# Optimization experiments

Measured on AMD Instinct MI355X. Metric: run time of the kernel, lower is better.

Reference implementation:

```python
import jax, jax.numpy as jnp
import numpy as np

N_R, N_S, D, L = 20000, 5000, 512, 3

def setup_inputs() -> dict:
    key = jax.random.key(0)
    ks = jax.random.split(key, 7)
    s = 1.0 / np.sqrt(D)  # xavier-ish scale to keep activations bounded
    return {
        "h_s": jax.random.normal(ks[0], (N_S, D), jnp.float32),
        "A_rs": jax.random.uniform(ks[1], (N_R, N_S), jnp.float32),
        "r_embed": jax.random.normal(ks[2], (N_R, D), jnp.float32) * s,
        "Wr": jax.random.normal(ks[3], (L, D, D), jnp.float32) * s,  # reading self-transform per layer
        "Ws": jax.random.normal(ks[4], (L, D, D), jnp.float32) * s,  # skill->reading cross-transform
        "Vr": jax.random.normal(ks[5], (L, D, D), jnp.float32) * s,  # reading->skill cross-transform
        "Vs": jax.random.normal(ks[6], (L, D, D), jnp.float32) * s,  # skill self-transform
    }

def reference(h_s, A_rs, r_embed, Wr, Ws, Vr, Vs):
    # ReadingGCNStage.forward: h = dropout(r_embed.weight) (eval-mode no-op),
    # then BipartiteGCNStack(h_s, h, A_rs): per-layer degree-normalized bipartite
    # message passing with dense per-side transforms and ReLU.
    eps = 1e-6
    deg_r = A_rs.sum(axis=1, keepdims=True) + eps   # [N_R, 1] reading degrees
    deg_s = A_rs.sum(axis=0)[:, None] + eps          # [N_S, 1] skill degrees
    h_r = r_embed
    for l in range(Wr.shape[0]):  # fixed small n_layers
        m_r = (A_rs @ h_s) / deg_r        # [N_R, D] mean-aggregated skill msgs
        m_s = (A_rs.T @ h_r) / deg_s      # [N_S, D] mean-aggregated reading msgs
        h_r_new = jax.nn.relu(m_r @ Ws[l] + h_r @ Wr[l])
        h_s = jax.nn.relu(m_s @ Vr[l] + h_s @ Vs[l])
        h_r = h_r_new
    return h_r  # updated reading embeddings [N_R, D]
```

## Files before the change

### kernel.cpp

```cpp
#include <hip/hip_runtime.h>


typedef __bf16 bf16_t;
typedef __attribute__((ext_vector_type(8))) __bf16 bf16x8;
typedef __attribute__((ext_vector_type(4))) __bf16 bf16x4;
typedef __attribute__((ext_vector_type(4))) float f32x4;

#define N_R 20000
#define N_S 5000
#define DD  512
#define MR_PAD 20224
#define MS_PAD 5120
#define KS_PAD 5056
#define KR_PAD 20224

__device__ __forceinline__ void gll16(const bf16_t* g, bf16_t* l) {
  __builtin_amdgcn_global_load_lds(
      (const __attribute__((address_space(1))) void*)g,
      (__attribute__((address_space(3))) void*)l, 16, 0, 0);
}


__global__ __launch_bounds__(256) void conv_rowsum_A(
    const float* __restrict__ A, bf16_t* __restrict__ Ab, float* __restrict__ deg_r) {
  int r = blockIdx.x;
  int t = threadIdx.x;
  __shared__ float wsum[4];
  if (r < N_R) {
    const float4* Arow = (const float4*)(A + (size_t)r * N_S);
    float s = 0.f;
    for (int c4 = t; c4 < N_S / 4; c4 += 256) {
      float4 v = Arow[c4];
      s += v.x + v.y + v.z + v.w;
      bf16x4 pv;
      pv[0] = (bf16_t)v.x; pv[1] = (bf16_t)v.y; pv[2] = (bf16_t)v.z; pv[3] = (bf16_t)v.w;
      *(bf16x4*)(Ab + (size_t)r * KS_PAD + 4 * c4) = pv;
    }
    if (t < KS_PAD - N_S) Ab[(size_t)r * KS_PAD + N_S + t] = (bf16_t)0.f;
    for (int off = 32; off > 0; off >>= 1) s += __shfl_down(s, off, 64);
    if ((t & 63) == 0) wsum[t >> 6] = s;
    __syncthreads();
    if (t == 0) deg_r[r] = wsum[0] + wsum[1] + wsum[2] + wsum[3] + 1e-6f;
  } else {
    for (int c = t; c < KS_PAD; c += 256) Ab[(size_t)r * KS_PAD + c] = (bf16_t)0.f;
  }
}

__global__ void init_deg_s(float* __restrict__ deg_s) {
  int i = blockIdx.x * 256 + threadIdx.x;
  if (i < N_S) deg_s[i] = 1e-6f;
}

__global__ __launch_bounds__(256) void transpose_A_deg(
    const bf16_t* __restrict__ Ab, bf16_t* __restrict__ At, float* __restrict__ deg_s) {
  __shared__ float tile[64][65];
  __shared__ float csum[4][64];
  int rt = blockIdx.x * 64;
  int st = blockIdx.y * 64;
  int tx = threadIdx.x & 63;
  int ty = threadIdx.x >> 6;
  int s = st + tx;
  float part = 0.f;
  for (int i = 0; i < 16; ++i) {
    int rr = ty * 16 + i;
    int r = rt + rr;
    float v = 0.f;
    if (r < N_R && s < KS_PAD) v = (float)Ab[(size_t)r * KS_PAD + s];
    tile[rr][tx] = v;
    part += v;
  }
  csum[ty][tx] = part;
  __syncthreads();
  if (ty == 0 && s < N_S)
    atomicAdd(&deg_s[s], csum[0][tx] + csum[1][tx] + csum[2][tx] + csum[3][tx]);
  for (int i = 0; i < 16; ++i) {
    int rr = ty * 16 + i;
    int r = rt + tx;
    if (r < KR_PAD) At[(size_t)(st + rr) * KR_PAD + r] = (bf16_t)tile[tx][rr];
  }
}

template <typename SrcT>
__global__ __launch_bounds__(256) void transpose_to_bf16(
    const SrcT* __restrict__ src, int R, int C, bf16_t* __restrict__ dst, int ldd) {
  __shared__ float tile[64][65];
  int rt = blockIdx.x * 64;
  int ct = blockIdx.y * 64;
  int tx = threadIdx.x & 63;
  int ty = threadIdx.x >> 6;
  for (int i = 0; i < 16; ++i) {
    int rr = ty * 16 + i;
    int r = rt + rr;
    float v = 0.f;
    if (r < R) v = (float)src[(size_t)r * C + ct + tx];
    tile[rr][tx] = v;
  }
  __syncthreads();
  for (int i = 0; i < 16; ++i) {
    int rr = ty * 16 + i;
    int r = rt + tx;
    if (r < ldd) dst[(size_t)(ct + rr) * ldd + r] = (bf16_t)tile[tx][rr];
  }
}

__global__ __launch_bounds__(256) void transpose_weights(
    const float* __restrict__ Wr, const float* __restrict__ Ws,
    const float* __restrict__ Vr, const float* __restrict__ Vs,
    bf16_t* __restrict__ WT) {
  int z = blockIdx.z;
  int t4 = z & 3, l = z >> 2;
  const float* srcs[4] = {Wr, Ws, Vr, Vs};
  const float* src = srcs[t4] + (size_t)l * DD * DD;
  bf16_t* dst = WT + (size_t)z * DD * DD;
  __shared__ float tile[64][65];
  int rt = blockIdx.x * 64, ct = blockIdx.y * 64;
  int tx = threadIdx.x & 63, ty = threadIdx.x >> 6;
  for (int i = 0; i < 16; ++i) {
    int rr = ty * 16 + i;
    tile[rr][tx] = src[(size_t)(rt + rr) * DD + ct + tx];
  }
  __syncthreads();
  for (int i = 0; i < 16; ++i) {
    int rr = ty * 16 + i;
    dst[(size_t)(ct + rr) * DD + rt + tx] = (bf16_t)tile[tx][rr];
  }
}

__global__ __launch_bounds__(256) void conv_pad(
    const float* __restrict__ src, bf16_t* __restrict__ dst, int R, int Rp) {
  size_t i = (size_t)blockIdx.x * 256 + threadIdx.x;
  size_t tot = (size_t)Rp * DD;
  if (i < tot) {
    int r = (int)(i / DD);
    dst[i] = (r < R) ? (bf16_t)src[i] : (bf16_t)0.f;
  }
}

__global__ __launch_bounds__(256) void combine_div(
    const float* __restrict__ part, int S, size_t stride,
    const float* __restrict__ deg, int Mreal, int Mpad, bf16_t* __restrict__ out) {
  size_t base = ((size_t)blockIdx.x * 256 + threadIdx.x) * 4;
  if (base >= (size_t)Mpad * DD) return;
  f32x4 s = *(const f32x4*)(part + base);
  for (int k = 1; k < S; ++k) s += *(const f32x4*)(part + (size_t)k * stride + base);
  int r = (int)(base >> 9);
  float inv = (r < Mreal) ? 1.0f / deg[r] : 0.f;
  bf16x4 o;
  o[0] = (bf16_t)(s[0] * inv); o[1] = (bf16_t)(s[1] * inv);
  o[2] = (bf16_t)(s[2] * inv); o[3] = (bf16_t)(s[3] * inv);
  *(bf16x4*)(out + base) = o;
}

__global__ __launch_bounds__(512, 2) void gemm256(
    const bf16_t* __restrict__ A, const bf16_t* __restrict__ B, int ld,
    int kt_total, int kt_chunk, float* __restrict__ Cpart, size_t part_stride) {
  __shared__ bf16_t As[2][256 * 64];
  __shared__ bf16_t Bs[2][256 * 64];
  const int tid = threadIdx.x;
  const int lane = tid & 63;
  const int wave = tid >> 6;
  const int bid = blockIdx.x;
  const int m0 = (bid >> 1) * 256;
  const int n0 = (bid & 1) * 256;
  const int z = blockIdx.y;
  const int ktb = z * kt_chunk;
  int kte = ktb + kt_chunk;
  if (kte > kt_total) kte = kt_total;
  if (ktb >= kte) return;
  const int wm = (wave >> 2) * 128;
  const int wn = (wave & 3) * 64;
  const int lr = lane & 15;
  const int quad = lane >> 4;
  const int rloc = lane >> 3;
  const int cel = ((lane & 7) ^ rloc) * 8;

  auto SA = [&](int b, int q, int t) {
    int k0 = (t < kte ? t : kte - 1) * 64;
    gll16(A + (size_t)(m0 + q * 64 + wave * 8 + rloc) * ld + k0 + cel,
          &As[b][(q * 64 + wave * 8) * 64]);
  };
  auto SB = [&](int b, int q, int t) {
    int k0 = (t < kte ? t : kte - 1) * 64;
    gll16(B + (size_t)(n0 + q * 64 + wave * 8 + rloc) * ld + k0 + cel,
          &Bs[b][(q * 64 + wave * 8) * 64]);
  };

  f32x4 acc[8][4] = {};
  bf16x8 af[4], bf[4];

#define PHASE(BUF, MH, KS, READB, ...)                                           \
  {                                                                              \
    _Pragma("unroll")                                                            \
    for (int i = 0; i < 4; ++i) {                                                \
      int r = wm + (MH) * 64 + i * 16 + lr;                                      \
      af[i] = *(const bf16x8*)&As[BUF][r * 64 +                                  \
                                       (((KS) * 32 + quad * 8) ^ ((r & 7) * 8))];\
    }                                                                            \
    if (READB) {                                                                 \
      _Pragma("unroll")                                                          \
      for (int j = 0; j < 4; ++j) {                                              \
        int r = wn + j * 16 + lr;                                                \
        bf[j] = *(const bf16x8*)&Bs[BUF][r * 64 +                                \
                                       (((KS) * 32 + quad * 8) ^ ((r & 7) * 8))];\
      }                                                                          \
    }                                                                            \
    __VA_ARGS__;                                                                 \
    __builtin_amdgcn_s_barrier();                                                \
    asm volatile("s_waitcnt lgkmcnt(0)" ::: "memory");                           \
    __builtin_amdgcn_s_setprio(1);                                               \
    _Pragma("unroll")                                                            \
    for (int i = 0; i < 4; ++i)                                                  \
      _Pragma("unroll")                                                          \
      for (int j = 0; j < 4; ++j)                                                \
        acc[(MH) * 4 + i][j] = __builtin_amdgcn_mfma_f32_16x16x32_bf16(          \
            af[i], bf[j], acc[(MH) * 4 + i][j], 0, 0, 0);                        \
    __builtin_amdgcn_s_setprio(0);                                               \
  }

  SB(0, 0, ktb); SB(0, 1, ktb); SB(0, 2, ktb); SB(0, 3, ktb);
  SA(0, 0, ktb); SA(0, 2, ktb);
  SA(0, 1, ktb); SA(0, 3, ktb);
  SB(1, 0, ktb + 1); SB(1, 1, ktb + 1);
  asm volatile("s_waitcnt vmcnt(4)" ::: "memory");
  __builtin_amdgcn_s_barrier();

  const int nt = kte - ktb;
  for (int ti = 0; ti < nt; ++ti) {
    const int t = ktb + ti;
    const int buf = ti & 1;
    const int nb = buf ^ 1;
    PHASE(buf, 0, 0, 1, SB(nb, 2, t + 1); SB(nb, 3, t + 1));
    asm volatile("s_waitcnt vmcnt(4)" ::: "memory");
    __builtin_amdgcn_s_barrier();
    PHASE(buf, 1, 0, 0, SA(nb, 0, t + 1); SA(nb, 2, t + 1));
    __builtin_amdgcn_s_barrier();
    PHASE(buf, 0, 1, 1, SA(nb, 1, t + 1); SA(nb, 3, t + 1));
    __builtin_amdgcn_s_barrier();
    PHASE(buf, 1, 1, 0, SB(buf, 0, t + 2); SB(buf, 1, t + 2));
    asm volatile("s_waitcnt vmcnt(4)" ::: "memory");
    __builtin_amdgcn_s_barrier();
  }
  asm volatile("s_waitcnt vmcnt(0)" ::: "memory");
#undef PHASE

  float* P = Cpart + (size_t)z * part_stride;
#pragma unroll
  for (int ii = 0; ii < 8; ++ii)
#pragma unroll
    for (int j = 0; j < 4; ++j) {
      int c = n0 + wn + j * 16 + lr;
#pragma unroll
      for (int g = 0; g < 4; ++g) {
        int r = m0 + wm + ii * 16 + quad * 4 + g;
        P[(size_t)r * DD + c] = acc[ii][j][g];
      }
    }
}

template <bool HAS2, int EPI>
__global__ __launch_bounds__(256) void gemm64(
    const bf16_t* __restrict__ A1, const bf16_t* __restrict__ B1, int kt1, int lda1, int ldb1,
    const bf16_t* __restrict__ A2, const bf16_t* __restrict__ B2, int kt2, int lda2, int ldb2,
    int kt_chunk,
    bf16_t* __restrict__ Cb, int Mreal, const float* __restrict__ deg,
    float* __restrict__ Cf, float* __restrict__ Cpart, size_t part_stride) {
  __shared__ bf16_t As[2 * 128 * 32];
  __shared__ bf16_t Bs[2 * 128 * 32];
  const int tid = threadIdx.x;
  const int lane = tid & 63;
  const int wave = tid >> 6;
  const int m0 = blockIdx.x * 128;
  const int n0 = blockIdx.y * 128;
  const int lrow = lane >> 2;
  const int lcol = (lane & 3) * 8;
  const int wm = (wave >> 1) * 64;
  const int wn = (wave & 1) * 64;
  const int lr = lane & 15;
  const int quad = lane >> 4;

  f32x4 acc[4][4] = {};

  const int ktot = kt1 + (HAS2 ? kt2 : 0);
  const int ktb = blockIdx.z * kt_chunk;
  const int kte = (ktb + kt_chunk < ktot) ? ktb + kt_chunk : ktot;

  for (int kt = ktb; kt < kte; ++kt) {
    const bf16_t* Ap; const bf16_t* Bp; int lda, ldb, k0;
    if (!HAS2 || kt < kt1) { Ap = A1; Bp = B1; lda = lda1; ldb = ldb1; k0 = kt * 64; }
    else                   { Ap = A2; Bp = B2; lda = lda2; ldb = ldb2; k0 = (kt - kt1) * 64; }
#pragma unroll
    for (int g = 0; g < 4; ++g) {
      const int h = g >> 1;
      const int rb = (g & 1) * 64 + wave * 16;
      gll16(Ap + (size_t)(m0 + rb + lrow) * lda + k0 + h * 32 + lcol,
            &As[h * 4096 + rb * 32]);
      gll16(Bp + (size_t)(n0 + rb + lrow) * ldb + k0 + h * 32 + lcol,
            &Bs[h * 4096 + rb * 32]);
    }
    __syncthreads();
    bf16x8 af[2][4], bq[2][4];
#pragma unroll
    for (int h = 0; h < 2; ++h)
#pragma unroll
      for (int i = 0; i < 4; ++i) {
        af[h][i] = *(const bf16x8*)&As[h * 4096 + (wm + i * 16 + lr) * 32 + quad * 8];
        bq[h][i] = *(const bf16x8*)&Bs[h * 4096 + (wn + i * 16 + lr) * 32 + quad * 8];
      }
#pragma unroll
    for (int h = 0; h < 2; ++h)
#pragma unroll
      for (int i = 0; i < 4; ++i)
#pragma unroll
        for (int j = 0; j < 4; ++j)
          acc[i][j] = __builtin_amdgcn_mfma_f32_16x16x32_bf16(af[h][i], bq[h][j], acc[i][j], 0, 0, 0);
    __syncthreads();
  }

  if (EPI == 2) {
    float* P = Cpart + blockIdx.z * part_stride;
#pragma unroll
    for (int i = 0; i < 4; ++i)
#pragma unroll
      for (int j = 0; j < 4; ++j) {
        int c = n0 + wn + j * 16 + lr;
#pragma unroll
        for (int g = 0; g < 4; ++g) {
          int r = m0 + wm + i * 16 + quad * 4 + g;
          P[(size_t)r * DD + c] = acc[i][j][g];
        }
      }
  } else {
#pragma unroll
    for (int i = 0; i < 4; ++i)
#pragma unroll
      for (int j = 0; j < 4; ++j) {
        int c = n0 + wn + j * 16 + lr;
#pragma unroll
        for (int g = 0; g < 4; ++g) {
          int r = m0 + wm + i * 16 + quad * 4 + g;
          if (r < Mreal) {
            float v = acc[i][j][g];
            if (EPI == 0) v /= deg[r];
            else v = fmaxf(v, 0.f);
            Cb[(size_t)r * DD + c] = (bf16_t)v;
            if (EPI == 1 && Cf != nullptr) Cf[(size_t)r * DD + c] = v;
          }
        }
      }
  }
}

extern "C" void kernel_launch(void* const* d_in, const int* in_sizes, int n_in,
                              void* d_out, int out_size, void* d_ws, size_t ws_size,
                              hipStream_t stream) {
  const float* h_s0 = (const float*)d_in[0];
  const float* A    = (const float*)d_in[1];
  const float* r_em = (const float*)d_in[2];
  const float* Wr   = (const float*)d_in[3];
  const float* Ws   = (const float*)d_in[4];
  const float* Vr   = (const float*)d_in[5];
  const float* Vs   = (const float*)d_in[6];
  float* out = (float*)d_out;

  char* p = (char*)d_ws;
  auto alloc = [&](size_t bytes) {
    char* q = p;
    p += (bytes + 255) & ~(size_t)255;
    return q;
  };
  bf16_t* Ab  = (bf16_t*)alloc((size_t)MR_PAD * KS_PAD * 2);
  bf16_t* At  = (bf16_t*)alloc((size_t)MS_PAD * KR_PAD * 2);
  bf16_t* hsT = (bf16_t*)alloc((size_t)DD * KS_PAD * 2);
  bf16_t* hrT = (bf16_t*)alloc((size_t)DD * KR_PAD * 2);
  bf16_t* WT  = (bf16_t*)alloc((size_t)12 * DD * DD * 2);
  bf16_t* hs_b[2] = {(bf16_t*)alloc((size_t)MS_PAD * DD * 2), (bf16_t*)alloc((size_t)MS_PAD * DD * 2)};
  bf16_t* hr_b[2] = {(bf16_t*)alloc((size_t)MR_PAD * DD * 2), (bf16_t*)alloc((size_t)MR_PAD * DD * 2)};
  bf16_t* mr_b = (bf16_t*)alloc((size_t)MR_PAD * DD * 2);
  bf16_t* ms_b = (bf16_t*)alloc((size_t)MS_PAD * DD * 2);
  float* deg_r = (float*)alloc((size_t)N_R * 4);
  float* deg_s = (float*)alloc((size_t)N_S * 4);
  size_t core_bytes = (size_t)(p - (char*)d_ws);
  size_t part_stride_r = (size_t)MR_PAD * DD;
  size_t part_stride_s = (size_t)MS_PAD * DD;
  size_t part_bytes = (part_stride_r * 3 > part_stride_s * 6 ? part_stride_r * 3 : part_stride_s * 6) * 4;
  bool split_ok = (core_bytes + part_bytes + 256 <= ws_size);
  float* part = split_ok ? (float*)alloc(part_bytes) : nullptr;
  if (core_bytes > ws_size) return;

  conv_rowsum_A<<<MR_PAD, 256, 0, stream>>>(A, Ab, deg_r);
  init_deg_s<<<(N_S + 255) / 256, 256, 0, stream>>>(deg_s);
  transpose_A_deg<<<dim3(316, 80), 256, 0, stream>>>(Ab, At, deg_s);
  transpose_to_bf16<float><<<dim3(79, 8), 256, 0, stream>>>(h_s0, N_S, DD, hsT, KS_PAD);
  transpose_to_bf16<float><<<dim3(316, 8), 256, 0, stream>>>(r_em, N_R, DD, hrT, KR_PAD);
  transpose_weights<<<dim3(8, 8, 12), 256, 0, stream>>>(Wr, Ws, Vr, Vs, WT);
  conv_pad<<<(MS_PAD * DD) / 256, 256, 0, stream>>>(h_s0, hs_b[0], N_S, MS_PAD);
  conv_pad<<<(MR_PAD * DD) / 256, 256, 0, stream>>>(r_em, hr_b[0], N_R, MR_PAD);

  const int ktA = KS_PAD / 64;
  const int ktT = KR_PAD / 64;

  int cur = 0;
  for (int l = 0; l < 3; ++l) {
    bf16_t* WrT = WT + ((size_t)l * 4 + 0) * DD * DD;
    bf16_t* WsT = WT + ((size_t)l * 4 + 1) * DD * DD;
    bf16_t* VrT = WT + ((size_t)l * 4 + 2) * DD * DD;
    bf16_t* VsT = WT + ((size_t)l * 4 + 3) * DD * DD;

    if (split_ok) {
      gemm256<<<dim3(79 * 2, 3), 512, 0, stream>>>(
          Ab, hsT, KS_PAD, ktA, 27, part, part_stride_r);
      combine_div<<<MR_PAD * DD / 1024, 256, 0, stream>>>(
          part, 3, part_stride_r, deg_r, N_R, MR_PAD, mr_b);
    } else {
      gemm64<false, 0><<<dim3(158, 4, 1), 256, 0, stream>>>(
          Ab, hsT, ktA, KS_PAD, KS_PAD, nullptr, nullptr, 0, 0, 0,
          ktA, mr_b, N_R, deg_r, nullptr, nullptr, 0);
    }
    if (l < 2) {
      if (split_ok) {
        gemm256<<<dim3(20 * 2, 6), 512, 0, stream>>>(
            At, hrT, KR_PAD, ktT, 53, part, part_stride_s);
        combine_div<<<MS_PAD * DD / 1024, 256, 0, stream>>>(
            part, 6, part_stride_s, deg_s, N_S, MS_PAD, ms_b);
      } else {
        gemm64<false, 0><<<dim3(40, 4, 1), 256, 0, stream>>>(
            At, hrT, ktT, KR_PAD, KR_PAD, nullptr, nullptr, 0, 0, 0,
            ktT, ms_b, N_S, deg_s, nullptr, nullptr, 0);
      }
    }
    gemm64<true, 1><<<dim3(158, 4, 1), 256, 0, stream>>>(
        mr_b, WsT, 8, DD, DD, hr_b[cur], WrT, 8, DD, DD,
        16, hr_b[1 - cur], N_R, nullptr, (l == 2) ? out : nullptr, nullptr, 0);
    if (l < 2) {
      gemm64<true, 1><<<dim3(40, 4, 1), 256, 0, stream>>>(
          ms_b, VrT, 8, DD, DD, hs_b[cur], VsT, 8, DD, DD,
          16, hs_b[1 - cur], N_S, nullptr, nullptr, nullptr, 0);
      transpose_to_bf16<bf16_t><<<dim3(316, 8), 256, 0, stream>>>(hr_b[1 - cur], N_R, DD, hrT, KR_PAD);
      transpose_to_bf16<bf16_t><<<dim3(79, 8), 256, 0, stream>>>(hs_b[1 - cur], N_S, DD, hsT, KS_PAD);
    }
    cur = 1 - cur;
  }
}
```

Baseline: 1.868 ms.

## Merge paired GEMM/transposes into combined launches and store split-K partials in bf16

Pairs the reading-side and skill-side work of each layer into single launches: one grouped split-K GEMM kernel, one combine kernel, one dual dense-transform GEMM, and one transpose kernel. This cuts launch count and lets the small skill-side work fill the GPU alongside the reading side. Split-K partials are now written as bf16 instead of fp32, halving partial traffic at some accuracy cost. The transposes are vectorised to 16-byte loads and stores, and the init and pad kernels are merged. The fallback path for small workspaces is removed.

```diff
diff --git a/kernel.cpp b/kernel.cpp
--- a/kernel.cpp
+++ b/kernel.cpp
@@ -46,61 +46,114 @@
   }
 }
 
-__global__ void init_deg_s(float* __restrict__ deg_s) {
-  int i = blockIdx.x * 256 + threadIdx.x;
-  if (i < N_S) deg_s[i] = 1e-6f;
+__global__ __launch_bounds__(256) void conv_pad2(
+    const float* __restrict__ r_em, bf16_t* __restrict__ hr0,
+    const float* __restrict__ h_s0, bf16_t* __restrict__ hs0,
+    float* __restrict__ deg_s) {
+  size_t i = (size_t)blockIdx.x * 256 + threadIdx.x;
+  const size_t totR = (size_t)MR_PAD * DD;
+  const size_t totS = (size_t)MS_PAD * DD;
+  if (i < totR) {
+    int r = (int)(i >> 9);
+    hr0[i] = (r < N_R) ? (bf16_t)r_em[i] : (bf16_t)0.f;
+  } else if (i < totR + totS) {
+    size_t j = i - totR;
+    int r = (int)(j >> 9);
+    hs0[j] = (r < N_S) ? (bf16_t)h_s0[j] : (bf16_t)0.f;
+  } else {
+    size_t j = i - totR - totS;
+    if (j < N_S) deg_s[j] = 1e-6f;
+  }
 }
 
 __global__ __launch_bounds__(256) void transpose_A_deg(
     const bf16_t* __restrict__ Ab, bf16_t* __restrict__ At, float* __restrict__ deg_s) {
   __shared__ float tile[64][65];
-  __shared__ float csum[4][64];
   int rt = blockIdx.x * 64;
   int st = blockIdx.y * 64;
-  int tx = threadIdx.x & 63;
-  int ty = threadIdx.x >> 6;
-  int s = st + tx;
-  float part = 0.f;
-  for (int i = 0; i < 16; ++i) {
-    int rr = ty * 16 + i;
+  int t = threadIdx.x;
+  const bool inA = (st < KS_PAD);
+  int row = t >> 3;
+  int c = (t & 7) * 8;
+#pragma unroll
+  for (int k = 0; k < 2; ++k) {
+    int rr = row + k * 32;
+    if (inA) {
+      bf16x8 v = *(const bf16x8*)(Ab + (size_t)(rt + rr) * KS_PAD + st + c);
+#pragma unroll
+      for (int j = 0; j < 8; ++j) tile[rr][c + j] = (float)v[j];
+    } else {
+#pragma unroll
+      for (int j = 0; j < 8; ++j) tile[rr][c + j] = 0.f;
+    }
+  }
+  __syncthreads();
+  if (t < 64 && inA && st + t < N_S) {
+    float s = 0.f;
+#pragma unroll 8
+    for (int r = 0; r < 64; ++r) s += tile[r][t];
+    atomicAdd(&deg_s[st + t], s);
+  }
+  int sl = t >> 2;
+  int r0 = (t & 3) * 16;
+  bf16x8 w0, w1;
+#pragma unroll
+  for (int i = 0; i < 8; ++i) w0[i] = (bf16_t)tile[r0 + i][sl];
+#pragma unroll
+  for (int i = 0; i < 8; ++i) w1[i] = (bf16_t)tile[r0 + 8 + i][sl];
+  *(bf16x8*)(At + (size_t)(st + sl) * KR_PAD + rt + r0) = w0;
+  *(bf16x8*)(At + (size_t)(st + sl) * KR_PAD + rt + r0 + 8) = w1;
+}
+
+__device__ __forceinline__ void load8f(const float* p, float* f) {
+  float4 a = *(const float4*)p;
+  float4 b = *(const float4*)(p + 4);
+  f[0] = a.x; f[1] = a.y; f[2] = a.z; f[3] = a.w;
+  f[4] = b.x; f[5] = b.y; f[6] = b.z; f[7] = b.w;
+}
+__device__ __forceinline__ void load8f(const bf16_t* p, float* f) {
+  bf16x8 v = *(const bf16x8*)p;
+#pragma unroll
+  for (int j = 0; j < 8; ++j) f[j] = (float)v[j];
+}
+
+template <typename SrcT>
+__global__ __launch_bounds__(256) void transpose2_to_bf16(
+    const SrcT* __restrict__ s1, int R1, bf16_t* __restrict__ d1, int ldd1, int nbx1, int nb1,
+    const SrcT* __restrict__ s2, int R2, bf16_t* __restrict__ d2, int ldd2, int nbx2) {
+  int bid = blockIdx.x;
+  const SrcT* src; int R; bf16_t* dst; int ldd, nbx;
+  if (bid < nb1) { src = s1; R = R1; dst = d1; ldd = ldd1; nbx = nbx1; }
+  else { bid -= nb1; src = s2; R = R2; dst = d2; ldd = ldd2; nbx = nbx2; }
+  int rt = (bid % nbx) * 64;
+  int ct = (bid / nbx) * 64;
+  __shared__ float tile[64][65];
+  int t = threadIdx.x;
+  int row = t >> 3;
+  int c = (t & 7) * 8;
+#pragma unroll
+  for (int k = 0; k < 2; ++k) {
+    int rr = row + k * 32;
     int r = rt + rr;
-    float v = 0.f;
-    if (r < N_R && s < KS_PAD) v = (float)Ab[(size_t)r * KS_PAD + s];
-    tile[rr][tx] = v;
-    part += v;
-  }
-  csum[ty][tx] = part;
+    float f[8];
+    if (r < R) load8f(src + (size_t)r * DD + ct + c, f);
+    else {
+#pragma unroll
+      for (int j = 0; j < 8; ++j) f[j] = 0.f;
+    }
+#pragma unroll
+    for (int j = 0; j < 8; ++j) tile[rr][c + j] = f[j];
+  }
   __syncthreads();
-  if (ty == 0 && s < N_S)
-    atomicAdd(&deg_s[s], csum[0][tx] + csum[1][tx] + csum[2][tx] + csum[3][tx]);
-  for (int i = 0; i < 16; ++i) {
-    int rr = ty * 16 + i;
-    int r = rt + tx;
-    if (r < KR_PAD) At[(size_t)(st + rr) * KR_PAD + r] = (bf16_t)tile[tx][rr];
-  }
-}
-
-template <typename SrcT>
-__global__ __launch_bounds__(256) void transpose_to_bf16(
-    const SrcT* __restrict__ src, int R, int C, bf16_t* __restrict__ dst, int ldd) {
-  __shared__ float tile[64][65];
-  int rt = blockIdx.x * 64;
-  int ct = blockIdx.y * 64;
-  int tx = threadIdx.x & 63;
-  int ty = threadIdx.x >> 6;
-  for (int i = 0; i < 16; ++i) {
-    int rr = ty * 16 + i;
-    int r = rt + rr;
-    float v = 0.f;
-    if (r < R) v = (float)src[(size_t)r * C + ct + tx];
-    tile[rr][tx] = v;
-  }
-  __syncthreads();
-  for (int i = 0; i < 16; ++i) {
-    int rr = ty * 16 + i;
-    int r = rt + tx;
-    if (r < ldd) dst[(size_t)(ct + rr) * ldd + r] = (bf16_t)tile[tx][rr];
-  }
+  int sl = t >> 2;
+  int r0 = (t & 3) * 16;
+  bf16x8 w0, w1;
+#pragma unroll
+  for (int i = 0; i < 8; ++i) w0[i] = (bf16_t)tile[r0 + i][sl];
+#pragma unroll
+  for (int i = 0; i < 8; ++i) w1[i] = (bf16_t)tile[r0 + 8 + i][sl];
+  *(bf16x8*)(dst + (size_t)(ct + sl) * ldd + rt + r0) = w0;
+  *(bf16x8*)(dst + (size_t)(ct + sl) * ldd + rt + r0 + 8) = w1;
 }
 
 __global__ __launch_bounds__(256) void transpose_weights(
@@ -126,47 +179,53 @@
   }
 }
 
-__global__ __launch_bounds__(256) void conv_pad(
-    const float* __restrict__ src, bf16_t* __restrict__ dst, int R, int Rp) {
-  size_t i = (size_t)blockIdx.x * 256 + threadIdx.x;
-  size_t tot = (size_t)Rp * DD;
-  if (i < tot) {
-    int r = (int)(i / DD);
-    dst[i] = (r < R) ? (bf16_t)src[i] : (bf16_t)0.f;
-  }
-}
-
-__global__ __launch_bounds__(256) void combine_div(
-    const float* __restrict__ part, int S, size_t stride,
-    const float* __restrict__ deg, int Mreal, int Mpad, bf16_t* __restrict__ out) {
-  size_t base = ((size_t)blockIdx.x * 256 + threadIdx.x) * 4;
-  if (base >= (size_t)Mpad * DD) return;
-  f32x4 s = *(const f32x4*)(part + base);
-  for (int k = 1; k < S; ++k) s += *(const f32x4*)(part + (size_t)k * stride + base);
+__global__ __launch_bounds__(256) void combine2(
+    const bf16_t* __restrict__ p1, int S1, size_t st1, const float* __restrict__ deg1,
+    int M1, bf16_t* __restrict__ o1, int nb1,
+    const bf16_t* __restrict__ p2, int S2, size_t st2, const float* __restrict__ deg2,
+    int M2, bf16_t* __restrict__ o2) {
+  int bid = blockIdx.x;
+  const bf16_t* p; int S; size_t st; const float* deg; int M; bf16_t* o;
+  if (bid < nb1) { p = p1; S = S1; st = st1; deg = deg1; M = M1; o = o1; }
+  else { bid -= nb1; p = p2; S = S2; st = st2; deg = deg2; M = M2; o = o2; }
+  size_t base = ((size_t)bid * 256 + threadIdx.x) * 8;
+  float acc[8] = {};
+  for (int k = 0; k < S; ++k) {
+    bf16x8 v = *(const bf16x8*)(p + (size_t)k * st + base);
+#pragma unroll
+    for (int j = 0; j < 8; ++j) acc[j] += (float)v[j];
+  }
   int r = (int)(base >> 9);
-  float inv = (r < Mreal) ? 1.0f / deg[r] : 0.f;
-  bf16x4 o;
-  o[0] = (bf16_t)(s[0] * inv); o[1] = (bf16_t)(s[1] * inv);
-  o[2] = (bf16_t)(s[2] * inv); o[3] = (bf16_t)(s[3] * inv);
-  *(bf16x4*)(out + base) = o;
-}
-
-__global__ __launch_bounds__(512, 2) void gemm256(
-    const bf16_t* __restrict__ A, const bf16_t* __restrict__ B, int ld,
-    int kt_total, int kt_chunk, float* __restrict__ Cpart, size_t part_stride) {
+  float inv = (r < M) ? 1.0f / deg[r] : 0.f;
+  bf16x8 w;
+#pragma unroll
+  for (int j = 0; j < 8; ++j) w[j] = (bf16_t)(acc[j] * inv);
+  *(bf16x8*)(o + base) = w;
+}
+
+__global__ __launch_bounds__(512, 2) void gemm256d(
+    const bf16_t* __restrict__ A1, const bf16_t* __restrict__ B1, int ld1,
+    int kt1, int chunk1, bf16_t* __restrict__ P1, size_t ps1, int nx1, int nb1,
+    const bf16_t* __restrict__ A2, const bf16_t* __restrict__ B2, int ld2,
+    int kt2, int chunk2, bf16_t* __restrict__ P2, size_t ps2, int nx2) {
   __shared__ bf16_t As[2][256 * 64];
   __shared__ bf16_t Bs[2][256 * 64];
+  int bid = blockIdx.x;
+  const bf16_t* A; const bf16_t* B; bf16_t* P;
+  int ld, kt_total, chunk, nx; size_t ps;
+  if (bid < nb1) { A = A1; B = B1; ld = ld1; kt_total = kt1; chunk = chunk1; P = P1; ps = ps1; nx = nx1; }
+  else { bid -= nb1; A = A2; B = B2; ld = ld2; kt_total = kt2; chunk = chunk2; P = P2; ps = ps2; nx = nx2; }
+  const int bx = bid % nx;
+  const int z  = bid / nx;
+  const int m0 = (bx >> 1) * 256;
+  const int n0 = (bx & 1) * 256;
+  const int ktb = z * chunk;
+  int kte = ktb + chunk;
+  if (kte > kt_total) kte = kt_total;
+  if (ktb >= kte) return;
   const int tid = threadIdx.x;
   const int lane = tid & 63;
   const int wave = tid >> 6;
-  const int bid = blockIdx.x;
-  const int m0 = (bid >> 1) * 256;
-  const int n0 = (bid & 1) * 256;
-  const int z = blockIdx.y;
-  const int ktb = z * kt_chunk;
-  int kte = ktb + kt_chunk;
-  if (kte > kt_total) kte = kt_total;
-  if (ktb >= kte) return;
   const int wm = (wave >> 2) * 128;
   const int wn = (wave & 3) * 64;
   const int lr = lane & 15;
@@ -243,7 +302,7 @@
   asm volatile("s_waitcnt vmcnt(0)" ::: "memory");
 #undef PHASE
 
-  float* P = Cpart + (size_t)z * part_stride;
+  bf16_t* Pz = P + (size_t)z * ps;
 #pragma unroll
   for (int ii = 0; ii < 8; ++ii)
 #pragma unroll
@@ -252,25 +311,29 @@
 #pragma unroll
       for (int g = 0; g < 4; ++g) {
         int r = m0 + wm + ii * 16 + quad * 4 + g;
-        P[(size_t)r * DD + c] = acc[ii][j][g];
+        Pz[(size_t)r * DD + c] = (bf16_t)acc[ii][j][g];
       }
     }
 }
 
-template <bool HAS2, int EPI>
-__global__ __launch_bounds__(256) void gemm64(
-    const bf16_t* __restrict__ A1, const bf16_t* __restrict__ B1, int kt1, int lda1, int ldb1,
-    const bf16_t* __restrict__ A2, const bf16_t* __restrict__ B2, int kt2, int lda2, int ldb2,
-    int kt_chunk,
-    bf16_t* __restrict__ Cb, int Mreal, const float* __restrict__ deg,
-    float* __restrict__ Cf, float* __restrict__ Cpart, size_t part_stride) {
+__global__ __launch_bounds__(256) void gemm64_dual(
+    const bf16_t* __restrict__ Aa1, const bf16_t* __restrict__ Ba1,
+    const bf16_t* __restrict__ Ab1, const bf16_t* __restrict__ Bb1,
+    bf16_t* __restrict__ C1, int M1, float* __restrict__ Cf1, int nx1, int nb1,
+    const bf16_t* __restrict__ Aa2, const bf16_t* __restrict__ Ba2,
+    const bf16_t* __restrict__ Ab2, const bf16_t* __restrict__ Bb2,
+    bf16_t* __restrict__ C2, int M2, int nx2) {
   __shared__ bf16_t As[2 * 128 * 32];
   __shared__ bf16_t Bs[2 * 128 * 32];
+  int bid = blockIdx.x;
+  const bf16_t *Aa, *Ba, *Abp, *Bb; bf16_t* C; float* Cf; int M, nx;
+  if (bid < nb1) { Aa = Aa1; Ba = Ba1; Abp = Ab1; Bb = Bb1; C = C1; M = M1; Cf = Cf1; nx = nx1; }
+  else { bid -= nb1; Aa = Aa2; Ba = Ba2; Abp = Ab2; Bb = Bb2; C = C2; M = M2; Cf = nullptr; nx = nx2; }
+  const int m0 = (bid % nx) * 128;
+  const int n0 = (bid / nx) * 128;
   const int tid = threadIdx.x;
   const int lane = tid & 63;
   const int wave = tid >> 6;
-  const int m0 = blockIdx.x * 128;
-  const int n0 = blockIdx.y * 128;
   const int lrow = lane >> 2;
   const int lcol = (lane & 3) * 8;
   const int wm = (wave >> 1) * 64;
@@ -280,21 +343,17 @@
 
   f32x4 acc[4][4] = {};
 
-  const int ktot = kt1 + (HAS2 ? kt2 : 0);
-  const int ktb = blockIdx.z * kt_chunk;
-  const int kte = (ktb + kt_chunk < ktot) ? ktb + kt_chunk : ktot;
-
-  for (int kt = ktb; kt < kte; ++kt) {
-    const bf16_t* Ap; const bf16_t* Bp; int lda, ldb, k0;
-    if (!HAS2 || kt < kt1) { Ap = A1; Bp = B1; lda = lda1; ldb = ldb1; k0 = kt * 64; }
-    else                   { Ap = A2; Bp = B2; lda = lda2; ldb = ldb2; k0 = (kt - kt1) * 64; }
+  for (int kt = 0; kt < 16; ++kt) {
+    const bf16_t* Ap = (kt < 8) ? Aa : Abp;
+    const bf16_t* Bp = (kt < 8) ? Ba : Bb;
+    const int k0 = (kt & 7) * 64;
 #pragma unroll
     for (int g = 0; g < 4; ++g) {
       const int h = g >> 1;
       const int rb = (g & 1) * 64 + wave * 16;
-      gll16(Ap + (size_t)(m0 + rb + lrow) * lda + k0 + h * 32 + lcol,
+      gll16(Ap + (size_t)(m0 + rb + lrow) * DD + k0 + h * 32 + lcol,
             &As[h * 4096 + rb * 32]);
-      gll16(Bp + (size_t)(n0 + rb + lrow) * ldb + k0 + h * 32 + lcol,
+      gll16(Bp + (size_t)(n0 + rb + lrow) * DD + k0 + h * 32 + lcol,
             &Bs[h * 4096 + rb * 32]);
     }
     __syncthreads();
@@ -316,38 +375,21 @@
     __syncthreads();
   }
 
-  if (EPI == 2) {
-    float* P = Cpart + blockIdx.z * part_stride;
-#pragma unroll
-    for (int i = 0; i < 4; ++i)
-#pragma unroll
-      for (int j = 0; j < 4; ++j) {
-        int c = n0 + wn + j * 16 + lr;
-#pragma unroll
-        for (int g = 0; g < 4; ++g) {
-          int r = m0 + wm + i * 16 + quad * 4 + g;
-          P[(size_t)r * DD + c] = acc[i][j][g];
+#pragma unroll
+  for (int i = 0; i < 4; ++i)
+#pragma unroll
+    for (int j = 0; j < 4; ++j) {
+      int c = n0 + wn + j * 16 + lr;
+#pragma unroll
+      for (int g = 0; g < 4; ++g) {
+        int r = m0 + wm + i * 16 + quad * 4 + g;
+        if (r < M) {
+          float v = fmaxf(acc[i][j][g], 0.f);
+          C[(size_t)r * DD + c] = (bf16_t)v;
+          if (Cf != nullptr) Cf[(size_t)r * DD + c] = v;
         }
       }
-  } else {
-#pragma unroll
-    for (int i = 0; i < 4; ++i)
-#pragma unroll
-      for (int j = 0; j < 4; ++j) {
-        int c = n0 + wn + j * 16 + lr;
-#pragma unroll
-        for (int g = 0; g < 4; ++g) {
-          int r = m0 + wm + i * 16 + quad * 4 + g;
-          if (r < Mreal) {
-            float v = acc[i][j][g];
-            if (EPI == 0) v /= deg[r];
-            else v = fmaxf(v, 0.f);
-            Cb[(size_t)r * DD + c] = (bf16_t)v;
-            if (EPI == 1 && Cf != nullptr) Cf[(size_t)r * DD + c] = v;
-          }
-        }
-      }
-  }
+    }
 }
 
 extern "C" void kernel_launch(void* const* d_in, const int* in_sizes, int n_in,
@@ -379,22 +421,22 @@
   bf16_t* ms_b = (bf16_t*)alloc((size_t)MS_PAD * DD * 2);
   float* deg_r = (float*)alloc((size_t)N_R * 4);
   float* deg_s = (float*)alloc((size_t)N_S * 4);
-  size_t core_bytes = (size_t)(p - (char*)d_ws);
-  size_t part_stride_r = (size_t)MR_PAD * DD;
-  size_t part_stride_s = (size_t)MS_PAD * DD;
-  size_t part_bytes = (part_stride_r * 3 > part_stride_s * 6 ? part_stride_r * 3 : part_stride_s * 6) * 4;
-  bool split_ok = (core_bytes + part_bytes + 256 <= ws_size);
-  float* part = split_ok ? (float*)alloc(part_bytes) : nullptr;
-  if (core_bytes > ws_size) return;
+  const size_t ps_r = (size_t)MR_PAD * DD;
+  const size_t ps_s = (size_t)MS_PAD * DD;
+  bf16_t* part_r = (bf16_t*)alloc(ps_r * 3 * 2);
+  bf16_t* part_s = (bf16_t*)alloc(ps_s * 7 * 2);
+  if ((size_t)(p - (char*)d_ws) > ws_size) return;
 
   conv_rowsum_A<<<MR_PAD, 256, 0, stream>>>(A, Ab, deg_r);
-  init_deg_s<<<(N_S + 255) / 256, 256, 0, stream>>>(deg_s);
+  {
+    size_t tot = (size_t)MR_PAD * DD + (size_t)MS_PAD * DD + N_S;
+    conv_pad2<<<(unsigned)((tot + 255) / 256), 256, 0, stream>>>(r_em, hr_b[0], h_s0, hs_b[0], deg_s);
+  }
   transpose_A_deg<<<dim3(316, 80), 256, 0, stream>>>(Ab, At, deg_s);
-  transpose_to_bf16<float><<<dim3(79, 8), 256, 0, stream>>>(h_s0, N_S, DD, hsT, KS_PAD);
-  transpose_to_bf16<float><<<dim3(316, 8), 256, 0, stream>>>(r_em, N_R, DD, hrT, KR_PAD);
+  transpose2_to_bf16<float><<<632 + 2528, 256, 0, stream>>>(
+      h_s0, N_S, hsT, KS_PAD, 79, 632,
+      r_em, N_R, hrT, KR_PAD, 316);
   transpose_weights<<<dim3(8, 8, 12), 256, 0, stream>>>(Wr, Ws, Vr, Vs, WT);
-  conv_pad<<<(MS_PAD * DD) / 256, 256, 0, stream>>>(h_s0, hs_b[0], N_S, MS_PAD);
-  conv_pad<<<(MR_PAD * DD) / 256, 256, 0, stream>>>(r_em, hr_b[0], N_R, MR_PAD);
 
   const int ktA = KS_PAD / 64;
   const int ktT = KR_PAD / 64;
@@ -406,37 +448,29 @@
     bf16_t* VrT = WT + ((size_t)l * 4 + 2) * DD * DD;
     bf16_t* VsT = WT + ((size_t)l * 4 + 3) * DD * DD;
 
-    if (split_ok) {
-      gemm256<<<dim3(79 * 2, 3), 512, 0, stream>>>(
-          Ab, hsT, KS_PAD, ktA, 27, part, part_stride_r);
-      combine_div<<<MR_PAD * DD / 1024, 256, 0, stream>>>(
-          part, 3, part_stride_r, deg_r, N_R, MR_PAD, mr_b);
+    if (l < 2) {
+      gemm256d<<<280 + 474, 512, 0, stream>>>(
+          At, hrT, KR_PAD, ktT, 46, part_s, ps_s, 40, 280,
+          Ab, hsT, KS_PAD, ktA, 27, part_r, ps_r, 158);
+      combine2<<<5056 + 1280, 256, 0, stream>>>(
+          part_r, 3, ps_r, deg_r, N_R, mr_b, 5056,
+          part_s, 7, ps_s, deg_s, N_S, ms_b);
+      gemm64_dual<<<632 + 160, 256, 0, stream>>>(
+          mr_b, WsT, hr_b[cur], WrT, hr_b[1 - cur], N_R, nullptr, 158, 632,
+          ms_b, VrT, hs_b[cur], VsT, hs_b[1 - cur], N_S, 40);
+      transpose2_to_bf16<bf16_t><<<2528 + 632, 256, 0, stream>>>(
+          hr_b[1 - cur], N_R, hrT, KR_PAD, 316, 2528,
+          hs_b[1 - cur], N_S, hsT, KS_PAD, 79);
     } else {
-      gemm64<false, 0><<<dim3(158, 4, 1), 256, 0, stream>>>(
-          Ab, hsT, ktA, KS_PAD, KS_PAD, nullptr, nullptr, 0, 0, 0,
-          ktA, mr_b, N_R, deg_r, nullptr, nullptr, 0);
-    }
-    if (l < 2) {
-      if (split_ok) {
-        gemm256<<<dim3(20 * 2, 6), 512, 0, stream>>>(
-            At, hrT, KR_PAD, ktT, 53, part, part_stride_s);
-        combine_div<<<MS_PAD * DD / 1024, 256, 0, stream>>>(
-            part, 6, part_stride_s, deg_s, N_S, MS_PAD, ms_b);
-      } else {
-        gemm64<false, 0><<<dim3(40, 4, 1), 256, 0, stream>>>(
-            At, hrT, ktT, KR_PAD, KR_PAD, nullptr, nullptr, 0, 0, 0,
-            ktT, ms_b, N_S, deg_s, nullptr, nullptr, 0);
-      }
-    }
-    gemm64<true, 1><<<dim3(158, 4, 1), 256, 0, stream>>>(
-        mr_b, WsT, 8, DD, DD, hr_b[cur], WrT, 8, DD, DD,
-        16, hr_b[1 - cur], N_R, nullptr, (l == 2) ? out : nullptr, nullptr, 0);
-    if (l < 2) {
-      gemm64<true, 1><<<dim3(40, 4, 1), 256, 0, stream>>>(
-          ms_b, VrT, 8, DD, DD, hs_b[cur], VsT, 8, DD, DD,
-          16, hs_b[1 - cur], N_S, nullptr, nullptr, nullptr, 0);
-      transpose_to_bf16<bf16_t><<<dim3(316, 8), 256, 0, stream>>>(hr_b[1 - cur], N_R, DD, hrT, KR_PAD);
-      transpose_to_bf16<bf16_t><<<dim3(79, 8), 256, 0, stream>>>(hs_b[1 - cur], N_S, DD, hsT, KS_PAD);
+      gemm256d<<<474, 512, 0, stream>>>(
+          Ab, hsT, KS_PAD, ktA, 27, part_r, ps_r, 158, 474,
+          Ab, hsT, KS_PAD, ktA, 27, part_r, ps_r, 158);
+      combine2<<<5056, 256, 0, stream>>>(
+          part_r, 3, ps_r, deg_r, N_R, mr_b, 5056,
+          part_r, 3, ps_r, deg_r, N_R, mr_b);
+      gemm64_dual<<<632, 256, 0, stream>>>(
+          mr_b, WsT, hr_b[cur], WrT, hr_b[1 - cur], N_R, out, 158, 632,
+          mr_b, WsT, hr_b[cur], WrT, hr_b[1 - cur], N_R, 158);
     }
     cur = 1 - cur;
   }
```

After: 1.651 ms. 1.13x faster.
